# Optimization experiments

Measured on AMD Instinct MI355X. Metric: run time of the kernel, lower is better.

Reference implementation:

```python
import jax, jax.numpy as jnp
import numpy as np

GRID_SIZE = 5
NUM_BASES = 2 ** GRID_SIZE - 1  # 31: actual number of Haar bases produced by the loop

def _haar_edges():
    left, mid, right = [], [], []
    for level in range(GRID_SIZE):
        scale = 2 ** level
        for shift in range(scale):
            left.append(shift / scale)
            mid.append((shift + 0.5) / scale)
            right.append((shift + 1.0) / scale)
    return (np.asarray(left, np.float32), np.asarray(mid, np.float32), np.asarray(right, np.float32))

_LEFT, _MID, _RIGHT = _haar_edges()


def setup_inputs() -> dict:
    key = jax.random.key(0)
    k1, k2, k3 = jax.random.split(key, 3)
    B, IN, OUT = 16384, 256, 256
    x = jax.random.normal(k1, (B, IN), dtype=jnp.float32)
    base_weight = jax.random.normal(k2, (OUT, IN), dtype=jnp.float32) * 0.05
    spline_weight = jax.random.normal(k3, (OUT, IN, NUM_BASES), dtype=jnp.float32) * 0.05
    spline_scaler = jnp.ones((OUT, IN), dtype=jnp.float32)
    return {"x": x, "base_weight": base_weight, "spline_weight": spline_weight, "spline_scaler": spline_scaler}


def reference(x, base_weight, spline_weight, spline_scaler):
    # per-feature min/max normalization over the batch dim
    x_min = jnp.min(x, axis=0, keepdims=True)
    x_max = jnp.max(x, axis=0, keepdims=True)
    xn = (x - x_min) / (x_max - x_min + 1e-8)            # [B, IN]
    left = jnp.asarray(_LEFT, x.dtype)
    mid = jnp.asarray(_MID, x.dtype)
    right = jnp.asarray(_RIGHT, x.dtype)
    xe = xn[..., None]                                    # [B, IN, 1]
    mask1 = ((xe >= left) & (xe < mid)).astype(x.dtype)
    mask2 = ((xe >= mid) & (xe < right)).astype(x.dtype)
    bases = mask1 - mask2                                 # [B, IN, NB]
    base_out = jax.nn.relu(x) @ base_weight.T             # [B, OUT]
    sw = spline_weight * spline_scaler[..., None]         # [OUT, IN, NB]
    wavelet_out = jnp.einsum('bik,oik->bo', bases, sw)    # [B, OUT]
    return base_out + wavelet_out
```

## Files before the change

### kernel.cpp

```cpp
#include <hip/hip_runtime.h>
#include <stdint.h>

typedef short s16x8 __attribute__((ext_vector_type(8)));
typedef float f32x4 __attribute__((ext_vector_type(4)));

#define IN_F   256
#define OUT_F  256
#define BATCH  16384
#define NB     31
#define KONE   8192
#define KTOT   8448

typedef const __attribute__((address_space(1))) void* as1cvp;
typedef __attribute__((address_space(3))) void* as3vp;

__device__ __forceinline__ unsigned short f2bf(float f) {
    unsigned u = __float_as_uint(f);
    u += 0x7FFFu + ((u >> 16) & 1u);
    return (unsigned short)(u >> 16);
}
__device__ __forceinline__ unsigned fkey(float f) {
    unsigned b = __float_as_uint(f);
    return (b & 0x80000000u) ? ~b : (b | 0x80000000u);
}
__device__ __forceinline__ float funkey(unsigned k) {
    return __uint_as_float((k & 0x80000000u) ? (k & 0x7FFFFFFFu) : ~k);
}

__global__ void minmax_atomic(const float* __restrict__ x,
                              unsigned* __restrict__ pminP, unsigned* __restrict__ pmaxP) {
    const int t = threadIdx.x;
    const int b0 = blockIdx.x * 128;
    float mn = 3.4e38f, mx = -3.4e38f;
    for (int r = 0; r < 128; ++r) {
        float v = x[(size_t)(b0 + r) * IN_F + t];
        mn = fminf(mn, v);
        mx = fmaxf(mx, v);
    }
    atomicMin(&pminP[t], fkey(mn));
    atomicMax(&pmaxP[t], fkey(mx));
}

__global__ void build_wb(const float* __restrict__ bw, const float* __restrict__ sw,
                         const float* __restrict__ sc, unsigned short* __restrict__ Wb) {
    const int o = blockIdx.x;
    const int t = threadIdx.x;
    for (int k = t; k < KTOT; k += 256) {
        float val;
        if (k < KONE) {
            int i = k >> 5, j = k & 31;
            float s = sc[o * IN_F + i];
            float acc = 0.f;
#pragma unroll
            for (int l = 0; l < 5; ++l) {
                int kk = (1 << l) - 1 + (j >> (5 - l));
                float w = sw[((size_t)(o * IN_F + i)) * NB + kk];
                acc += (((j >> (4 - l)) & 1) ? -w : w);
            }
            val = acc * s;
        } else {
            val = bw[o * IN_F + (k - KONE)];
        }
        Wb[(size_t)o * KTOT + k] = f2bf(val);
    }
}

__global__ __launch_bounds__(256) void leafk_t(
    const float* __restrict__ x, const unsigned* __restrict__ pminP,
    const unsigned* __restrict__ pmaxP, unsigned char* __restrict__ lt) {
    __shared__ unsigned char lsh[256 * 128];
    __shared__ float xminsh[IN_F], rdensh[IN_F];
    const int t = threadIdx.x;
    const int b0 = blockIdx.x * 128;
    {
        float mn = funkey(pminP[t]), mx = funkey(pmaxP[t]);
        xminsh[t] = mn;
        rdensh[t] = 1.0f / (mx - mn + 1e-8f);
    }
    __syncthreads();
    const float xmn = xminsh[t], rdn = rdensh[t];
    for (int r = 0; r < 128; ++r) {
        float v = x[(size_t)(b0 + r) * IN_F + t];
        float xn = (v - xmn) * rdn;
        int l = (int)(xn * 32.0f);
        lsh[t * 128 + r] = (l >= 0 && l < 32) ? (unsigned char)l : (unsigned char)255;
    }
    __syncthreads();
    const int lane = t & 63, w = t >> 6;
    const unsigned* lshU = (const unsigned*)lsh;
#pragma unroll
    for (int ib = 0; ib < 32; ++ib) {
        int i = ib * 8 + w * 2 + (lane >> 5);
        unsigned val = lshU[i * 32 + (lane & 31)];
        *(unsigned*)(lt + (size_t)i * BATCH + b0 + (lane & 31) * 4) = val;
    }
}

__global__ __launch_bounds__(64, 4) void gemm_kan(
    const float* __restrict__ x,
    const unsigned short* __restrict__ Wb,
    const unsigned char* __restrict__ lt,
    float* __restrict__ out)
{
    __shared__ unsigned short Ash[64 * 64];
    __shared__ unsigned short Bsh[2 * 64 * 64];

    const int lane  = threadIdx.x;
    const int mtile = blockIdx.x;
    const int ntile = blockIdx.y;

    {
        uint4 z; z.x = z.y = z.z = z.w = 0u;
        uint4* a4 = (uint4*)Ash;
#pragma unroll
        for (int r = 0; r < 8; ++r) a4[lane + r * 64] = z;
    }

    const unsigned char* bbase = (const unsigned char*)(Wb
        + (size_t)(ntile * 64 + (lane >> 3)) * KTOT
        + (((lane & 7) ^ (lane >> 3)) << 3));

    const int am0 = lane >> 1, am1 = 32 + (lane >> 1), ag = lane & 1;
    const size_t lrow0 = (size_t)mtile * 64;
    int ps0 = -1, ps1 = -1;

    unsigned char lf0 = lt[(size_t)ag * BATCH + lrow0 + am0];
    unsigned char lf1 = lt[(size_t)ag * BATCH + lrow0 + am1];

#pragma unroll
    for (int q = 0; q < 8; ++q)
        __builtin_amdgcn_global_load_lds(
            (as1cvp)(bbase + (size_t)q * 8 * KTOT * 2),
            (as3vp)(uint32_t)(uintptr_t)(Bsh + q * 512), 16, 0, 0);
    __syncthreads();

    f32x4 acc[4][4] = {};
    const int rr = lane & 15, kq = lane >> 4;

    for (int kb = 0; kb < 132; ++kb) {
        const int cur = kb & 1;
        if (kb < 128) {
            if (ps0 >= 0) Ash[ps0] = 0;
            if (ps1 >= 0) Ash[ps1] = 0;
            int l0 = lf0, l1 = lf1;
            if (l0 < 32) {
                int c = (ag << 2) + (l0 >> 3);
                ps0 = (am0 << 6) + ((c ^ (am0 & 7)) << 3) + (l0 & 7);
                Ash[ps0] = 0x3F80;
            } else ps0 = -1;
            if (l1 < 32) {
                int c = (ag << 2) + (l1 >> 3);
                ps1 = (am1 << 6) + ((c ^ (am1 & 7)) << 3) + (l1 & 7);
                Ash[ps1] = 0x3F80;
            } else ps1 = -1;
        } else {
            const float* xr = x + (size_t)(mtile * 64) * IN_F + (kb - 128) * 64 + lane;
            const int cslot = ((lane >> 3));
#pragma unroll
            for (int m = 0; m < 64; ++m) {
                float v = xr[(size_t)m * IN_F];
                Ash[(m << 6) + ((cslot ^ (m & 7)) << 3) + (lane & 7)] = f2bf(fmaxf(v, 0.0f));
            }
        }
        __syncthreads();

        if (kb + 1 < 132) {
            const unsigned char* src = bbase + (size_t)(kb + 1) * 128;
            unsigned short* dst = Bsh + (1 - cur) * 4096;
#pragma unroll
            for (int q = 0; q < 8; ++q)
                __builtin_amdgcn_global_load_lds(
                    (as1cvp)(src + (size_t)q * 8 * KTOT * 2),
                    (as3vp)(uint32_t)(uintptr_t)(dst + q * 512), 16, 0, 0);
        }
        if (kb + 1 < 128) {
            size_t lo = (size_t)((kb + 1) * 2 + ag) * BATCH + lrow0;
            lf0 = lt[lo + am0];
            lf1 = lt[lo + am1];
        }

        const unsigned short* bb = Bsh + cur * 4096;
#pragma unroll
        for (int ks = 0; ks < 2; ++ks) {
            const int c = (ks << 2) + kq;
            s16x8 af[4], bfr[4];
#pragma unroll
            for (int mt = 0; mt < 4; ++mt) {
                int m = mt * 16 + rr;
                af[mt] = *(const s16x8*)&Ash[(m << 6) + ((c ^ (m & 7)) << 3)];
            }
#pragma unroll
            for (int nt = 0; nt < 4; ++nt) {
                int n = nt * 16 + rr;
                bfr[nt] = *(const s16x8*)&bb[(n << 6) + ((c ^ (n & 7)) << 3)];
            }
#pragma unroll
            for (int mt = 0; mt < 4; ++mt)
#pragma unroll
                for (int nt = 0; nt < 4; ++nt)
                    acc[mt][nt] = __builtin_amdgcn_mfma_f32_16x16x32_bf16(
                        af[mt], bfr[nt], acc[mt][nt], 0, 0, 0);
        }
        __syncthreads();
    }

    const int rq = lane >> 4;
#pragma unroll
    for (int mt = 0; mt < 4; ++mt)
#pragma unroll
        for (int nt = 0; nt < 4; ++nt)
#pragma unroll
            for (int v = 0; v < 4; ++v) {
                int row = mtile * 64 + mt * 16 + rq * 4 + v;
                int col = ntile * 64 + nt * 16 + rr;
                out[(size_t)row * OUT_F + col] = acc[mt][nt][v];
            }
}

extern "C" void kernel_launch(void* const* d_in, const int* in_sizes, int n_in,
                              void* d_out, int out_size, void* d_ws, size_t ws_size,
                              hipStream_t stream) {
    (void)in_sizes; (void)n_in; (void)out_size; (void)ws_size;
    const float* x  = (const float*)d_in[0];
    const float* bw = (const float*)d_in[1];
    const float* sw = (const float*)d_in[2];
    const float* sc = (const float*)d_in[3];
    float* out = (float*)d_out;

    char* ws = (char*)d_ws;
    unsigned short* Wb   = (unsigned short*)ws;
    unsigned char*  lt   = (unsigned char*)(ws + 4325376);
    unsigned*       pminP = (unsigned*)(ws + 8519680);
    unsigned*       pmaxP = (unsigned*)(ws + 8520704);

    hipMemsetAsync(pminP, 0xFF, 1024, stream);
    hipMemsetAsync(pmaxP, 0x00, 1024, stream);

    minmax_atomic<<<128, 256, 0, stream>>>(x, pminP, pmaxP);
    build_wb<<<256, 256, 0, stream>>>(bw, sw, sc, Wb);
    leafk_t<<<128, 256, 0, stream>>>(x, pminP, pmaxP, lt);
    gemm_kan<<<dim3(256, 4), 64, 0, stream>>>(x, Wb, lt, out);
}
```

Baseline: 200.8 us.

## Split GEMM tile across two waves and widen grids of prep kernels

The GEMM block grows from one wave to two. Each wave computes 32 rows of the 64x64 tile, loads half the B tile, and sets one one-hot entry per K-step instead of two. The min/max, weight-build and leaf-transpose kernels now run on more blocks with smaller per-block work, which raises parallelism across the GPU's CUs. In exchange there are more blocks, more atomics, and the two waves must synchronise within a block.

```diff
diff --git a/kernel.cpp b/kernel.cpp
--- a/kernel.cpp
+++ b/kernel.cpp
@@ -30,9 +30,9 @@
 __global__ void minmax_atomic(const float* __restrict__ x,
                               unsigned* __restrict__ pminP, unsigned* __restrict__ pmaxP) {
     const int t = threadIdx.x;
-    const int b0 = blockIdx.x * 128;
+    const int b0 = blockIdx.x * 32;
     float mn = 3.4e38f, mx = -3.4e38f;
-    for (int r = 0; r < 128; ++r) {
+    for (int r = 0; r < 32; ++r) {
         float v = x[(size_t)(b0 + r) * IN_F + t];
         mn = fminf(mn, v);
         mx = fmaxf(mx, v);
@@ -44,8 +44,9 @@
 __global__ void build_wb(const float* __restrict__ bw, const float* __restrict__ sw,
                          const float* __restrict__ sc, unsigned short* __restrict__ Wb) {
     const int o = blockIdx.x;
+    const int k0 = blockIdx.y * 2112;
     const int t = threadIdx.x;
-    for (int k = t; k < KTOT; k += 256) {
+    for (int k = k0 + t; k < k0 + 2112; k += 256) {
         float val;
         if (k < KONE) {
             int i = k >> 5, j = k & 31;
@@ -68,10 +69,10 @@
 __global__ __launch_bounds__(256) void leafk_t(
     const float* __restrict__ x, const unsigned* __restrict__ pminP,
     const unsigned* __restrict__ pmaxP, unsigned char* __restrict__ lt) {
-    __shared__ unsigned char lsh[256 * 128];
+    __shared__ unsigned char lsh[256 * 68];
     __shared__ float xminsh[IN_F], rdensh[IN_F];
     const int t = threadIdx.x;
-    const int b0 = blockIdx.x * 128;
+    const int b0 = blockIdx.x * 64;
     {
         float mn = funkey(pminP[t]), mx = funkey(pmaxP[t]);
         xminsh[t] = mn;
@@ -79,24 +80,24 @@
     }
     __syncthreads();
     const float xmn = xminsh[t], rdn = rdensh[t];
-    for (int r = 0; r < 128; ++r) {
+    for (int r = 0; r < 64; ++r) {
         float v = x[(size_t)(b0 + r) * IN_F + t];
         float xn = (v - xmn) * rdn;
         int l = (int)(xn * 32.0f);
-        lsh[t * 128 + r] = (l >= 0 && l < 32) ? (unsigned char)l : (unsigned char)255;
+        lsh[t * 68 + r] = (l >= 0 && l < 32) ? (unsigned char)l : (unsigned char)255;
     }
     __syncthreads();
     const int lane = t & 63, w = t >> 6;
     const unsigned* lshU = (const unsigned*)lsh;
 #pragma unroll
-    for (int ib = 0; ib < 32; ++ib) {
-        int i = ib * 8 + w * 2 + (lane >> 5);
-        unsigned val = lshU[i * 32 + (lane & 31)];
-        *(unsigned*)(lt + (size_t)i * BATCH + b0 + (lane & 31) * 4) = val;
-    }
-}
-
-__global__ __launch_bounds__(64, 4) void gemm_kan(
+    for (int ib = 0; ib < 16; ++ib) {
+        int i = ib * 16 + w * 4 + (lane >> 4);
+        unsigned val = lshU[i * 17 + (lane & 15)];
+        *(unsigned*)(lt + (size_t)i * BATCH + b0 + (lane & 15) * 4) = val;
+    }
+}
+
+__global__ __launch_bounds__(128, 2) void gemm_kan(
     const float* __restrict__ x,
     const unsigned short* __restrict__ Wb,
     const unsigned char* __restrict__ lt,
@@ -105,7 +106,9 @@
     __shared__ unsigned short Ash[64 * 64];
     __shared__ unsigned short Bsh[2 * 64 * 64];
 
-    const int lane  = threadIdx.x;
+    const int t     = threadIdx.x;
+    const int lane  = t & 63;
+    const int wv    = t >> 6;
     const int mtile = blockIdx.x;
     const int ntile = blockIdx.y;
 
@@ -113,52 +116,47 @@
         uint4 z; z.x = z.y = z.z = z.w = 0u;
         uint4* a4 = (uint4*)Ash;
 #pragma unroll
-        for (int r = 0; r < 8; ++r) a4[lane + r * 64] = z;
+        for (int r = 0; r < 4; ++r) a4[t + r * 128] = z;
     }
 
     const unsigned char* bbase = (const unsigned char*)(Wb
-        + (size_t)(ntile * 64 + (lane >> 3)) * KTOT
+        + (size_t)(ntile * 64 + wv * 32 + (lane >> 3)) * KTOT
         + (((lane & 7) ^ (lane >> 3)) << 3));
 
-    const int am0 = lane >> 1, am1 = 32 + (lane >> 1), ag = lane & 1;
+    const int am = t >> 1;
+    const int ag = t & 1;
     const size_t lrow0 = (size_t)mtile * 64;
-    int ps0 = -1, ps1 = -1;
-
-    unsigned char lf0 = lt[(size_t)ag * BATCH + lrow0 + am0];
-    unsigned char lf1 = lt[(size_t)ag * BATCH + lrow0 + am1];
-
-#pragma unroll
-    for (int q = 0; q < 8; ++q)
+    int ps = -1;
+
+    unsigned char lf = lt[(size_t)ag * BATCH + lrow0 + am];
+
+#pragma unroll
+    for (int q = 0; q < 4; ++q)
         __builtin_amdgcn_global_load_lds(
             (as1cvp)(bbase + (size_t)q * 8 * KTOT * 2),
-            (as3vp)(uint32_t)(uintptr_t)(Bsh + q * 512), 16, 0, 0);
+            (as3vp)(uint32_t)(uintptr_t)(Bsh + wv * 2048 + q * 512), 16, 0, 0);
     __syncthreads();
 
-    f32x4 acc[4][4] = {};
+    f32x4 acc[2][4] = {};
     const int rr = lane & 15, kq = lane >> 4;
 
     for (int kb = 0; kb < 132; ++kb) {
         const int cur = kb & 1;
         if (kb < 128) {
-            if (ps0 >= 0) Ash[ps0] = 0;
-            if (ps1 >= 0) Ash[ps1] = 0;
-            int l0 = lf0, l1 = lf1;
-            if (l0 < 32) {
-                int c = (ag << 2) + (l0 >> 3);
-                ps0 = (am0 << 6) + ((c ^ (am0 & 7)) << 3) + (l0 & 7);
-                Ash[ps0] = 0x3F80;
-            } else ps0 = -1;
-            if (l1 < 32) {
-                int c = (ag << 2) + (l1 >> 3);
-                ps1 = (am1 << 6) + ((c ^ (am1 & 7)) << 3) + (l1 & 7);
-                Ash[ps1] = 0x3F80;
-            } else ps1 = -1;
+            if (ps >= 0) Ash[ps] = 0;
+            int l = lf;
+            if (l < 32) {
+                int c = (ag << 2) + (l >> 3);
+                ps = (am << 6) + ((c ^ (am & 7)) << 3) + (l & 7);
+                Ash[ps] = 0x3F80;
+            } else ps = -1;
         } else {
-            const float* xr = x + (size_t)(mtile * 64) * IN_F + (kb - 128) * 64 + lane;
-            const int cslot = ((lane >> 3));
-#pragma unroll
-            for (int m = 0; m < 64; ++m) {
-                float v = xr[(size_t)m * IN_F];
+            const float* xr = x + (size_t)(mtile * 64 + wv * 32) * IN_F + (kb - 128) * 64 + lane;
+            const int cslot = (lane >> 3);
+#pragma unroll
+            for (int m0 = 0; m0 < 32; ++m0) {
+                int m = wv * 32 + m0;
+                float v = xr[(size_t)m0 * IN_F];
                 Ash[(m << 6) + ((cslot ^ (m & 7)) << 3) + (lane & 7)] = f2bf(fmaxf(v, 0.0f));
             }
         }
@@ -166,27 +164,25 @@
 
         if (kb + 1 < 132) {
             const unsigned char* src = bbase + (size_t)(kb + 1) * 128;
-            unsigned short* dst = Bsh + (1 - cur) * 4096;
-#pragma unroll
-            for (int q = 0; q < 8; ++q)
+            unsigned short* dst = Bsh + (1 - cur) * 4096 + wv * 2048;
+#pragma unroll
+            for (int q = 0; q < 4; ++q)
                 __builtin_amdgcn_global_load_lds(
                     (as1cvp)(src + (size_t)q * 8 * KTOT * 2),
                     (as3vp)(uint32_t)(uintptr_t)(dst + q * 512), 16, 0, 0);
         }
         if (kb + 1 < 128) {
-            size_t lo = (size_t)((kb + 1) * 2 + ag) * BATCH + lrow0;
-            lf0 = lt[lo + am0];
-            lf1 = lt[lo + am1];
+            lf = lt[(size_t)((kb + 1) * 2 + ag) * BATCH + lrow0 + am];
         }
 
         const unsigned short* bb = Bsh + cur * 4096;
 #pragma unroll
         for (int ks = 0; ks < 2; ++ks) {
             const int c = (ks << 2) + kq;
-            s16x8 af[4], bfr[4];
-#pragma unroll
-            for (int mt = 0; mt < 4; ++mt) {
-                int m = mt * 16 + rr;
+            s16x8 af[2], bfr[4];
+#pragma unroll
+            for (int mt = 0; mt < 2; ++mt) {
+                int m = wv * 32 + mt * 16 + rr;
                 af[mt] = *(const s16x8*)&Ash[(m << 6) + ((c ^ (m & 7)) << 3)];
             }
 #pragma unroll
@@ -195,7 +191,7 @@
                 bfr[nt] = *(const s16x8*)&bb[(n << 6) + ((c ^ (n & 7)) << 3)];
             }
 #pragma unroll
-            for (int mt = 0; mt < 4; ++mt)
+            for (int mt = 0; mt < 2; ++mt)
 #pragma unroll
                 for (int nt = 0; nt < 4; ++nt)
                     acc[mt][nt] = __builtin_amdgcn_mfma_f32_16x16x32_bf16(
@@ -206,12 +202,12 @@
 
     const int rq = lane >> 4;
 #pragma unroll
-    for (int mt = 0; mt < 4; ++mt)
+    for (int mt = 0; mt < 2; ++mt)
 #pragma unroll
         for (int nt = 0; nt < 4; ++nt)
 #pragma unroll
             for (int v = 0; v < 4; ++v) {
-                int row = mtile * 64 + mt * 16 + rq * 4 + v;
+                int row = mtile * 64 + wv * 32 + mt * 16 + rq * 4 + v;
                 int col = ntile * 64 + nt * 16 + rr;
                 out[(size_t)row * OUT_F + col] = acc[mt][nt][v];
             }
@@ -236,8 +232,8 @@
     hipMemsetAsync(pminP, 0xFF, 1024, stream);
     hipMemsetAsync(pmaxP, 0x00, 1024, stream);
 
-    minmax_atomic<<<128, 256, 0, stream>>>(x, pminP, pmaxP);
-    build_wb<<<256, 256, 0, stream>>>(bw, sw, sc, Wb);
-    leafk_t<<<128, 256, 0, stream>>>(x, pminP, pmaxP, lt);
-    gemm_kan<<<dim3(256, 4), 64, 0, stream>>>(x, Wb, lt, out);
-}
+    minmax_atomic<<<512, 256, 0, stream>>>(x, pminP, pmaxP);
+    build_wb<<<dim3(256, 4), 256, 0, stream>>>(bw, sw, sc, Wb);
+    leafk_t<<<256, 256, 0, stream>>>(x, pminP, pmaxP, lt);
+    gemm_kan<<<dim3(256, 4), 128, 0, stream>>>(x, Wb, lt, out);
+}
```

Result: faster. 179.6 us (-10.6%).
